# Kernel tuning notes

Measured on AMD Instinct MI355X. Metric: run time of the kernel, lower is better.

Reference implementation:

```python
import jax, jax.numpy as jnp
import numpy as np

B, S, H = 1024, 512, 768
D1, D2 = 128, 1


def setup_inputs() -> dict:
    key = jax.random.key(0)
    k_feat, k_start, k_len, k_w1, k_w2 = jax.random.split(key, 5)
    features_extract = jax.random.normal(k_feat, (B, S, H), dtype=jnp.float32)
    start_token_idx = jax.random.randint(k_start, (B,), 1, 200, dtype=jnp.int64)
    span_len = jax.random.randint(k_len, (B,), 1, 65, dtype=jnp.int64)
    end_token_idx = start_token_idx + span_len  # guaranteed start < end <= 264 < S
    W1 = jax.random.normal(k_w1, (2 * H, D1), dtype=jnp.float32) * (1.0 / np.sqrt(2 * H))
    b1 = jnp.zeros((D1,), dtype=jnp.float32)
    W2 = jax.random.normal(k_w2, (D1, D2), dtype=jnp.float32) * (1.0 / np.sqrt(D1))
    b2 = jnp.zeros((D2,), dtype=jnp.float32)
    return {
        "features_extract": features_extract,
        "start_token_idx": start_token_idx,
        "end_token_idx": end_token_idx,
        "W1": W1, "b1": b1, "W2": W2, "b2": b2,
    }


def reference(features_extract, start_token_idx, end_token_idx, W1, b1, W2, b2):
    # CLS feature: token 0 of each example -> [B, 1, H]
    features_cls = features_extract[:, 0, :][:, None, :]

    # Ragged span mean-pool (vectorized replacement for the per-example loop):
    # mask[b, s] = start[b] <= s < end[b]
    pos = jnp.arange(features_extract.shape[1])  # [S]
    mask = (pos[None, :] >= start_token_idx[:, None]) & (pos[None, :] < end_token_idx[:, None])
    maskf = mask.astype(features_extract.dtype)  # [B, S]
    span_sum = jnp.einsum('bsh,bs->bh', features_extract, maskf)
    span_len = (end_token_idx - start_token_idx).astype(features_extract.dtype)  # >= 1
    features_crc = (span_sum / span_len[:, None])[:, None, :]  # [B, 1, H]

    # Concat + MLP head (dropout layers are identity in eval)
    features = jnp.concatenate([features_cls, features_crc], axis=2)  # [B, 1, 2H]
    h = jax.nn.relu(jnp.einsum('bid,dk->bik', features, W1) + b1)
    out = jax.nn.sigmoid(jnp.einsum('bik,ko->bio', h, W2) + b2)  # [B, 1, 1]
    return out
```

## Files before the change

kernel.cpp:

```cpp
#include <hip/hip_runtime.h>
#include <math.h>

constexpr int Bn = 1024;
constexpr int S  = 512;
constexpr int H  = 768;
constexpr int D1 = 128;
constexpr int HV = H / 4;
constexpr int NH = 512;


__global__ __launch_bounds__(256) void fused_pool_clshead(
    const float* __restrict__ feat, const int* __restrict__ start,
    const int* __restrict__ endp, float* __restrict__ gp,
    const float* __restrict__ W1, float* __restrict__ P) {
  __shared__ __align__(16) char smem[12288];

  const int t = threadIdx.x;

  if (blockIdx.x < NH) {
    float (*g)[384] = reinterpret_cast<float (*)[384]>(smem);
    float (*part)[4][D1] = reinterpret_cast<float (*)[4][D1]>(smem + 6144);

    const int c = blockIdx.x & 1;
    const int e0 = (blockIdx.x >> 1) * 4;
    const int dglob0 = c * 384;

    for (int i = t; i < 384; i += 256) {
      const int e = i / 96;
      const int j = i % 96;
      float4 v = *reinterpret_cast<const float4*>(
          feat + (size_t)(e0 + e) * S * H + dglob0 + j * 4);
      reinterpret_cast<float4*>(&g[e][0])[j] = v;
    }
    __syncthreads();

    const int k = t & (D1 - 1);
    const int sub = t >> 7;
    const int gofs = sub * 192;
    const float* Wc = W1 + (size_t)(dglob0 + gofs) * D1 + k;

    float a0 = 0.f, a1 = 0.f, a2 = 0.f, a3 = 0.f;
    #pragma unroll 4
    for (int d = 0; d < 192; d += 4) {
      float w0 = Wc[(size_t)(d + 0) * D1];
      float w1 = Wc[(size_t)(d + 1) * D1];
      float w2 = Wc[(size_t)(d + 2) * D1];
      float w3 = Wc[(size_t)(d + 3) * D1];
      float4 g0 = *reinterpret_cast<const float4*>(&g[0][gofs + d]);
      float4 g1 = *reinterpret_cast<const float4*>(&g[1][gofs + d]);
      float4 g2 = *reinterpret_cast<const float4*>(&g[2][gofs + d]);
      float4 g3 = *reinterpret_cast<const float4*>(&g[3][gofs + d]);
      a0 += g0.x * w0 + g0.y * w1 + g0.z * w2 + g0.w * w3;
      a1 += g1.x * w0 + g1.y * w1 + g1.z * w2 + g1.w * w3;
      a2 += g2.x * w0 + g2.y * w1 + g2.z * w2 + g2.w * w3;
      a3 += g3.x * w0 + g3.y * w1 + g3.z * w2 + g3.w * w3;
    }
    part[sub][0][k] = a0;
    part[sub][1][k] = a1;
    part[sub][2][k] = a2;
    part[sub][3][k] = a3;
    __syncthreads();

    if (t < D1) {
      #pragma unroll
      for (int e = 0; e < 4; ++e) {
        P[((size_t)c * Bn + (e0 + e)) * D1 + t] = part[0][e][t] + part[1][e][t];
      }
    }
    return;
  }

  {
    float4 (*pacc)[3][64] = reinterpret_cast<float4 (*)[3][64]>(smem);
    const int b = blockIdx.x - NH;
    const int w = t >> 6;
    const int l = t & 63;
    const float4* base =
        reinterpret_cast<const float4*>(feat) + (size_t)b * (S * HV);

    const int s0 = start[b];
    const int s1 = endp[b];

    float4 c0{0,0,0,0}, c1{0,0,0,0}, c2{0,0,0,0};
    float4 d0{0,0,0,0}, d1{0,0,0,0}, d2{0,0,0,0};
    int s = s0 + w;
    for (; s + 4 < s1; s += 8) {
      const float4* r0 = base + (size_t)s * HV;
      const float4* r1 = base + (size_t)(s + 4) * HV;
      float4 u0 = r0[l], u1 = r0[l + 64], u2 = r0[l + 128];
      float4 v0 = r1[l], v1 = r1[l + 64], v2 = r1[l + 128];
      c0.x += u0.x; c0.y += u0.y; c0.z += u0.z; c0.w += u0.w;
      c1.x += u1.x; c1.y += u1.y; c1.z += u1.z; c1.w += u1.w;
      c2.x += u2.x; c2.y += u2.y; c2.z += u2.z; c2.w += u2.w;
      d0.x += v0.x; d0.y += v0.y; d0.z += v0.z; d0.w += v0.w;
      d1.x += v1.x; d1.y += v1.y; d1.z += v1.z; d1.w += v1.w;
      d2.x += v2.x; d2.y += v2.y; d2.z += v2.z; d2.w += v2.w;
    }
    for (; s < s1; s += 4) {
      const float4* r0 = base + (size_t)s * HV;
      float4 u0 = r0[l], u1 = r0[l + 64], u2 = r0[l + 128];
      c0.x += u0.x; c0.y += u0.y; c0.z += u0.z; c0.w += u0.w;
      c1.x += u1.x; c1.y += u1.y; c1.z += u1.z; c1.w += u1.w;
      c2.x += u2.x; c2.y += u2.y; c2.z += u2.z; c2.w += u2.w;
    }
    c0.x += d0.x; c0.y += d0.y; c0.z += d0.z; c0.w += d0.w;
    c1.x += d1.x; c1.y += d1.y; c1.z += d1.z; c1.w += d1.w;
    c2.x += d2.x; c2.y += d2.y; c2.z += d2.z; c2.w += d2.w;
    pacc[w][0][l] = c0;
    pacc[w][1][l] = c1;
    pacc[w][2][l] = c2;
    __syncthreads();

    if (t < 192) {
      const int seg = t >> 6, ln = t & 63;
      float4 a = pacc[0][seg][ln], bb = pacc[1][seg][ln];
      float4 cq = pacc[2][seg][ln], dq = pacc[3][seg][ln];
      const float inv = 1.0f / (float)(s1 - s0);
      float4 r;
      r.x = ((a.x + bb.x) + (cq.x + dq.x)) * inv;
      r.y = ((a.y + bb.y) + (cq.y + dq.y)) * inv;
      r.z = ((a.z + bb.z) + (cq.z + dq.z)) * inv;
      r.w = ((a.w + bb.w) + (cq.w + dq.w)) * inv;
      reinterpret_cast<float4*>(gp)[(size_t)b * HV + t] = r;
    }
  }
}

__global__ __launch_bounds__(256) void crc_head(
    const float* __restrict__ gp, const float* __restrict__ W1,
    float* __restrict__ P) {
  __shared__ float g[4][192];
  __shared__ float part[2][4][D1];

  const int t = threadIdx.x;
  const int cc = blockIdx.x & 3;
  const int e0 = (blockIdx.x >> 2) * 4;
  const int dd04 = cc * 48;

  if (t < 192) {
    const int e = t / 48;
    const int j = t % 48;
    float4 v = reinterpret_cast<const float4*>(gp)[(size_t)(e0 + e) * HV + dd04 + j];
    reinterpret_cast<float4*>(&g[e][0])[j] = v;
  }
  __syncthreads();

  const int k = t & (D1 - 1);
  const int sub = t >> 7;
  const int gofs = sub * 96;
  const float* Wc = W1 + (size_t)(H + cc * 192 + gofs) * D1 + k;

  float a0 = 0.f, a1 = 0.f, a2 = 0.f, a3 = 0.f;
  #pragma unroll 2
  for (int d = 0; d < 96; d += 8) {
    float w0 = Wc[(size_t)(d + 0) * D1];
    float w1 = Wc[(size_t)(d + 1) * D1];
    float w2 = Wc[(size_t)(d + 2) * D1];
    float w3 = Wc[(size_t)(d + 3) * D1];
    float w4 = Wc[(size_t)(d + 4) * D1];
    float w5 = Wc[(size_t)(d + 5) * D1];
    float w6 = Wc[(size_t)(d + 6) * D1];
    float w7 = Wc[(size_t)(d + 7) * D1];
    #define ACC8(i)                                                        \
    {                                                                      \
      float4 gA = *reinterpret_cast<const float4*>(&g[i][gofs + d]);       \
      float4 gB = *reinterpret_cast<const float4*>(&g[i][gofs + d + 4]);   \
      a##i += gA.x * w0 + gA.y * w1 + gA.z * w2 + gA.w * w3                \
            + gB.x * w4 + gB.y * w5 + gB.z * w6 + gB.w * w7;               \
    }
    ACC8(0) ACC8(1) ACC8(2) ACC8(3)
    #undef ACC8
  }
  part[sub][0][k] = a0;
  part[sub][1][k] = a1;
  part[sub][2][k] = a2;
  part[sub][3][k] = a3;
  __syncthreads();

  if (t < D1) {
    #pragma unroll
    for (int e = 0; e < 4; ++e) {
      P[((size_t)(2 + cc) * Bn + (e0 + e)) * D1 + t] =
          part[0][e][t] + part[1][e][t];
    }
  }
}

__global__ __launch_bounds__(256) void finalize(
    const float* __restrict__ P, const float* __restrict__ b1,
    const float* __restrict__ W2, const float* __restrict__ b2,
    float* __restrict__ out) {
  const int t = threadIdx.x;
  const int w = t >> 6, l = t & 63;
  const int e = blockIdx.x * 4 + w;
  const int k0 = l, k1 = l + 64;
  float h0 = b1[k0], h1 = b1[k1];
  #pragma unroll
  for (int c = 0; c < 6; ++c) {
    h0 += P[((size_t)c * Bn + e) * D1 + k0];
    h1 += P[((size_t)c * Bn + e) * D1 + k1];
  }
  h0 = fmaxf(h0, 0.f); h1 = fmaxf(h1, 0.f);
  float v = h0 * W2[k0] + h1 * W2[k1];
  #pragma unroll
  for (int off = 32; off > 0; off >>= 1) v += __shfl_down(v, off);
  if (l == 0) out[e] = 1.0f / (1.0f + expf(-(v + b2[0])));
}

extern "C" void kernel_launch(void* const* d_in, const int* in_sizes, int n_in,
                              void* d_out, int out_size, void* d_ws, size_t ws_size,
                              hipStream_t stream) {
  const float* feat = (const float*)d_in[0];
  const int* start  = (const int*)d_in[1];
  const int* endp   = (const int*)d_in[2];
  const float* W1   = (const float*)d_in[3];
  const float* b1   = (const float*)d_in[4];
  const float* W2   = (const float*)d_in[5];
  const float* b2   = (const float*)d_in[6];
  float* out = (float*)d_out;

  float* wsf = (float*)d_ws;
  float* gp  = wsf;
  float* P   = gp + (size_t)Bn * H;

  hipLaunchKernelGGL(fused_pool_clshead, dim3(NH + Bn), dim3(256), 0,
                     stream, feat, start, endp, gp, W1, P);
  hipLaunchKernelGGL(crc_head, dim3(Bn), dim3(256), 0, stream, gp, W1, P);
  hipLaunchKernelGGL(finalize, dim3(Bn / 4), dim3(256), 0, stream,
                     P, b1, W2, b2, out);
}
```

Measured before the change: 32.85 us.

## Pipeline pooling halves with head and finalize stages across four kernels

Splits the pooling work into two halves by example and co-schedules the second half of pooling with the CRC head for the first half. The CRC head for the second half then runs alongside finalize for the first half, and a last kernel finalizes the rest. The aim is to hide the small, latency-bound head and finalize kernels behind bandwidth-bound pooling instead of running them serially. The cost is an extra kernel launch and some load imbalance between the mixed block types.

Result: slower. 36.44 us (+10.9%).

```diff
diff --git a/kernel.cpp b/kernel.cpp
--- a/kernel.cpp
+++ b/kernel.cpp
@@ -6,141 +6,135 @@
 constexpr int H  = 768;
 constexpr int D1 = 128;
 constexpr int HV = H / 4;
-constexpr int NH = 512;
-
-
-__global__ __launch_bounds__(256) void fused_pool_clshead(
+constexpr int HALF = 512;
+
+
+
+__device__ __forceinline__ void cls_head_fn(
+    const float* __restrict__ feat, const float* __restrict__ W1,
+    float* __restrict__ P, int bid, int t, char* smem) {
+  float (*g)[384] = reinterpret_cast<float (*)[384]>(smem);
+  float (*part)[4][D1] = reinterpret_cast<float (*)[4][D1]>(smem + 6144);
+
+  const int c = bid & 1;
+  const int e0 = (bid >> 1) * 4;
+  const int dglob0 = c * 384;
+
+  for (int i = t; i < 384; i += 256) {
+    const int e = i / 96;
+    const int j = i % 96;
+    float4 v = *reinterpret_cast<const float4*>(
+        feat + (size_t)(e0 + e) * S * H + dglob0 + j * 4);
+    reinterpret_cast<float4*>(&g[e][0])[j] = v;
+  }
+  __syncthreads();
+
+  const int k = t & (D1 - 1);
+  const int sub = t >> 7;
+  const int gofs = sub * 192;
+  const float* Wc = W1 + (size_t)(dglob0 + gofs) * D1 + k;
+
+  float a0 = 0.f, a1 = 0.f, a2 = 0.f, a3 = 0.f;
+  #pragma unroll 4
+  for (int d = 0; d < 192; d += 4) {
+    float w0 = Wc[(size_t)(d + 0) * D1];
+    float w1 = Wc[(size_t)(d + 1) * D1];
+    float w2 = Wc[(size_t)(d + 2) * D1];
+    float w3 = Wc[(size_t)(d + 3) * D1];
+    float4 g0 = *reinterpret_cast<const float4*>(&g[0][gofs + d]);
+    float4 g1 = *reinterpret_cast<const float4*>(&g[1][gofs + d]);
+    float4 g2 = *reinterpret_cast<const float4*>(&g[2][gofs + d]);
+    float4 g3 = *reinterpret_cast<const float4*>(&g[3][gofs + d]);
+    a0 += g0.x * w0 + g0.y * w1 + g0.z * w2 + g0.w * w3;
+    a1 += g1.x * w0 + g1.y * w1 + g1.z * w2 + g1.w * w3;
+    a2 += g2.x * w0 + g2.y * w1 + g2.z * w2 + g2.w * w3;
+    a3 += g3.x * w0 + g3.y * w1 + g3.z * w2 + g3.w * w3;
+  }
+  part[sub][0][k] = a0;
+  part[sub][1][k] = a1;
+  part[sub][2][k] = a2;
+  part[sub][3][k] = a3;
+  __syncthreads();
+
+  if (t < D1) {
+    #pragma unroll
+    for (int e = 0; e < 4; ++e) {
+      P[((size_t)c * Bn + (e0 + e)) * D1 + t] = part[0][e][t] + part[1][e][t];
+    }
+  }
+}
+
+__device__ __forceinline__ void pool_fn(
     const float* __restrict__ feat, const int* __restrict__ start,
-    const int* __restrict__ endp, float* __restrict__ gp,
-    const float* __restrict__ W1, float* __restrict__ P) {
-  __shared__ __align__(16) char smem[12288];
-
-  const int t = threadIdx.x;
-
-  if (blockIdx.x < NH) {
-    float (*g)[384] = reinterpret_cast<float (*)[384]>(smem);
-    float (*part)[4][D1] = reinterpret_cast<float (*)[4][D1]>(smem + 6144);
-
-    const int c = blockIdx.x & 1;
-    const int e0 = (blockIdx.x >> 1) * 4;
-    const int dglob0 = c * 384;
-
-    for (int i = t; i < 384; i += 256) {
-      const int e = i / 96;
-      const int j = i % 96;
-      float4 v = *reinterpret_cast<const float4*>(
-          feat + (size_t)(e0 + e) * S * H + dglob0 + j * 4);
-      reinterpret_cast<float4*>(&g[e][0])[j] = v;
-    }
-    __syncthreads();
-
-    const int k = t & (D1 - 1);
-    const int sub = t >> 7;
-    const int gofs = sub * 192;
-    const float* Wc = W1 + (size_t)(dglob0 + gofs) * D1 + k;
-
-    float a0 = 0.f, a1 = 0.f, a2 = 0.f, a3 = 0.f;
-    #pragma unroll 4
-    for (int d = 0; d < 192; d += 4) {
-      float w0 = Wc[(size_t)(d + 0) * D1];
-      float w1 = Wc[(size_t)(d + 1) * D1];
-      float w2 = Wc[(size_t)(d + 2) * D1];
-      float w3 = Wc[(size_t)(d + 3) * D1];
-      float4 g0 = *reinterpret_cast<const float4*>(&g[0][gofs + d]);
-      float4 g1 = *reinterpret_cast<const float4*>(&g[1][gofs + d]);
-      float4 g2 = *reinterpret_cast<const float4*>(&g[2][gofs + d]);
-      float4 g3 = *reinterpret_cast<const float4*>(&g[3][gofs + d]);
-      a0 += g0.x * w0 + g0.y * w1 + g0.z * w2 + g0.w * w3;
-      a1 += g1.x * w0 + g1.y * w1 + g1.z * w2 + g1.w * w3;
-      a2 += g2.x * w0 + g2.y * w1 + g2.z * w2 + g2.w * w3;
-      a3 += g3.x * w0 + g3.y * w1 + g3.z * w2 + g3.w * w3;
-    }
-    part[sub][0][k] = a0;
-    part[sub][1][k] = a1;
-    part[sub][2][k] = a2;
-    part[sub][3][k] = a3;
-    __syncthreads();
-
-    if (t < D1) {
-      #pragma unroll
-      for (int e = 0; e < 4; ++e) {
-        P[((size_t)c * Bn + (e0 + e)) * D1 + t] = part[0][e][t] + part[1][e][t];
-      }
-    }
-    return;
-  }
-
-  {
-    float4 (*pacc)[3][64] = reinterpret_cast<float4 (*)[3][64]>(smem);
-    const int b = blockIdx.x - NH;
-    const int w = t >> 6;
-    const int l = t & 63;
-    const float4* base =
-        reinterpret_cast<const float4*>(feat) + (size_t)b * (S * HV);
-
-    const int s0 = start[b];
-    const int s1 = endp[b];
-
-    float4 c0{0,0,0,0}, c1{0,0,0,0}, c2{0,0,0,0};
-    float4 d0{0,0,0,0}, d1{0,0,0,0}, d2{0,0,0,0};
-    int s = s0 + w;
-    for (; s + 4 < s1; s += 8) {
-      const float4* r0 = base + (size_t)s * HV;
-      const float4* r1 = base + (size_t)(s + 4) * HV;
-      float4 u0 = r0[l], u1 = r0[l + 64], u2 = r0[l + 128];
-      float4 v0 = r1[l], v1 = r1[l + 64], v2 = r1[l + 128];
-      c0.x += u0.x; c0.y += u0.y; c0.z += u0.z; c0.w += u0.w;
-      c1.x += u1.x; c1.y += u1.y; c1.z += u1.z; c1.w += u1.w;
-      c2.x += u2.x; c2.y += u2.y; c2.z += u2.z; c2.w += u2.w;
-      d0.x += v0.x; d0.y += v0.y; d0.z += v0.z; d0.w += v0.w;
-      d1.x += v1.x; d1.y += v1.y; d1.z += v1.z; d1.w += v1.w;
-      d2.x += v2.x; d2.y += v2.y; d2.z += v2.z; d2.w += v2.w;
-    }
-    for (; s < s1; s += 4) {
-      const float4* r0 = base + (size_t)s * HV;
-      float4 u0 = r0[l], u1 = r0[l + 64], u2 = r0[l + 128];
-      c0.x += u0.x; c0.y += u0.y; c0.z += u0.z; c0.w += u0.w;
-      c1.x += u1.x; c1.y += u1.y; c1.z += u1.z; c1.w += u1.w;
-      c2.x += u2.x; c2.y += u2.y; c2.z += u2.z; c2.w += u2.w;
-    }
-    c0.x += d0.x; c0.y += d0.y; c0.z += d0.z; c0.w += d0.w;
-    c1.x += d1.x; c1.y += d1.y; c1.z += d1.z; c1.w += d1.w;
-    c2.x += d2.x; c2.y += d2.y; c2.z += d2.z; c2.w += d2.w;
-    pacc[w][0][l] = c0;
-    pacc[w][1][l] = c1;
-    pacc[w][2][l] = c2;
-    __syncthreads();
-
-    if (t < 192) {
-      const int seg = t >> 6, ln = t & 63;
-      float4 a = pacc[0][seg][ln], bb = pacc[1][seg][ln];
-      float4 cq = pacc[2][seg][ln], dq = pacc[3][seg][ln];
-      const float inv = 1.0f / (float)(s1 - s0);
-      float4 r;
-      r.x = ((a.x + bb.x) + (cq.x + dq.x)) * inv;
-      r.y = ((a.y + bb.y) + (cq.y + dq.y)) * inv;
-      r.z = ((a.z + bb.z) + (cq.z + dq.z)) * inv;
-      r.w = ((a.w + bb.w) + (cq.w + dq.w)) * inv;
-      reinterpret_cast<float4*>(gp)[(size_t)b * HV + t] = r;
-    }
-  }
-}
-
-__global__ __launch_bounds__(256) void crc_head(
+    const int* __restrict__ endp, float* __restrict__ gp, int b, int t,
+    char* smem) {
+  float4 (*pacc)[3][64] = reinterpret_cast<float4 (*)[3][64]>(smem);
+  const int w = t >> 6;
+  const int l = t & 63;
+  const float4* base =
+      reinterpret_cast<const float4*>(feat) + (size_t)b * (S * HV);
+
+  const int s0 = start[b];
+  const int s1 = endp[b];
+
+  float4 c0{0,0,0,0}, c1{0,0,0,0}, c2{0,0,0,0};
+  float4 d0{0,0,0,0}, d1{0,0,0,0}, d2{0,0,0,0};
+  int s = s0 + w;
+  for (; s + 4 < s1; s += 8) {
+    const float4* r0 = base + (size_t)s * HV;
+    const float4* r1 = base + (size_t)(s + 4) * HV;
+    float4 u0 = r0[l], u1 = r0[l + 64], u2 = r0[l + 128];
+    float4 v0 = r1[l], v1 = r1[l + 64], v2 = r1[l + 128];
+    c0.x += u0.x; c0.y += u0.y; c0.z += u0.z; c0.w += u0.w;
+    c1.x += u1.x; c1.y += u1.y; c1.z += u1.z; c1.w += u1.w;
+    c2.x += u2.x; c2.y += u2.y; c2.z += u2.z; c2.w += u2.w;
+    d0.x += v0.x; d0.y += v0.y; d0.z += v0.z; d0.w += v0.w;
+    d1.x += v1.x; d1.y += v1.y; d1.z += v1.z; d1.w += v1.w;
+    d2.x += v2.x; d2.y += v2.y; d2.z += v2.z; d2.w += v2.w;
+  }
+  for (; s < s1; s += 4) {
+    const float4* r0 = base + (size_t)s * HV;
+    float4 u0 = r0[l], u1 = r0[l + 64], u2 = r0[l + 128];
+    c0.x += u0.x; c0.y += u0.y; c0.z += u0.z; c0.w += u0.w;
+    c1.x += u1.x; c1.y += u1.y; c1.z += u1.z; c1.w += u1.w;
+    c2.x += u2.x; c2.y += u2.y; c2.z += u2.z; c2.w += u2.w;
+  }
+  c0.x += d0.x; c0.y += d0.y; c0.z += d0.z; c0.w += d0.w;
+  c1.x += d1.x; c1.y += d1.y; c1.z += d1.z; c1.w += d1.w;
+  c2.x += d2.x; c2.y += d2.y; c2.z += d2.z; c2.w += d2.w;
+  pacc[w][0][l] = c0;
+  pacc[w][1][l] = c1;
+  pacc[w][2][l] = c2;
+  __syncthreads();
+
+  if (t < 192) {
+    const int seg = t >> 6, ln = t & 63;
+    float4 a = pacc[0][seg][ln], bb = pacc[1][seg][ln];
+    float4 cq = pacc[2][seg][ln], dq = pacc[3][seg][ln];
+    const float inv = 1.0f / (float)(s1 - s0);
+    float4 r;
+    r.x = ((a.x + bb.x) + (cq.x + dq.x)) * inv;
+    r.y = ((a.y + bb.y) + (cq.y + dq.y)) * inv;
+    r.z = ((a.z + bb.z) + (cq.z + dq.z)) * inv;
+    r.w = ((a.w + bb.w) + (cq.w + dq.w)) * inv;
+    reinterpret_cast<float4*>(gp)[(size_t)b * HV + t] = r;
+  }
+}
+
+__device__ __forceinline__ void crc_fn(
     const float* __restrict__ gp, const float* __restrict__ W1,
-    float* __restrict__ P) {
-  __shared__ float g[4][192];
-  __shared__ float part[2][4][D1];
-
-  const int t = threadIdx.x;
-  const int cc = blockIdx.x & 3;
-  const int e0 = (blockIdx.x >> 2) * 4;
+    float* __restrict__ P, int cc, int eg, int t, char* smem) {
+  float (*g)[192] = reinterpret_cast<float (*)[192]>(smem);
+  float (*part)[4][D1] = reinterpret_cast<float (*)[4][D1]>(smem + 3072);
+
+  const int e0 = eg * 4;
   const int dd04 = cc * 48;
 
   if (t < 192) {
     const int e = t / 48;
     const int j = t % 48;
-    float4 v = reinterpret_cast<const float4*>(gp)[(size_t)(e0 + e) * HV + dd04 + j];
+    float4 v =
+        reinterpret_cast<const float4*>(gp)[(size_t)(e0 + e) * HV + dd04 + j];
     reinterpret_cast<float4*>(&g[e][0])[j] = v;
   }
   __syncthreads();
@@ -186,13 +180,12 @@
   }
 }
 
-__global__ __launch_bounds__(256) void finalize(
+__device__ __forceinline__ void fin_fn(
     const float* __restrict__ P, const float* __restrict__ b1,
     const float* __restrict__ W2, const float* __restrict__ b2,
-    float* __restrict__ out) {
-  const int t = threadIdx.x;
+    float* __restrict__ out, int e0, int t) {
   const int w = t >> 6, l = t & 63;
-  const int e = blockIdx.x * 4 + w;
+  const int e = e0 + w;
   const int k0 = l, k1 = l + 64;
   float h0 = b1[k0], h1 = b1[k1];
   #pragma unroll
@@ -205,6 +198,53 @@
   #pragma unroll
   for (int off = 32; off > 0; off >>= 1) v += __shfl_down(v, off);
   if (l == 0) out[e] = 1.0f / (1.0f + expf(-(v + b2[0])));
+}
+
+
+__global__ __launch_bounds__(256) void stage1(
+    const float* __restrict__ feat, const int* __restrict__ start,
+    const int* __restrict__ endp, float* __restrict__ gp,
+    const float* __restrict__ W1, float* __restrict__ P) {
+  __shared__ __align__(16) char smem[12288];
+  if (blockIdx.x < 512) {
+    cls_head_fn(feat, W1, P, blockIdx.x, threadIdx.x, smem);
+  } else {
+    pool_fn(feat, start, endp, gp, blockIdx.x - 512, threadIdx.x, smem);
+  }
+}
+
+__global__ __launch_bounds__(256) void stage2(
+    const float* __restrict__ feat, const int* __restrict__ start,
+    const int* __restrict__ endp, float* __restrict__ gp,
+    const float* __restrict__ W1, float* __restrict__ P) {
+  __shared__ __align__(16) char smem[12288];
+  if (blockIdx.x < 512) {
+    crc_fn(gp, W1, P, blockIdx.x & 3, blockIdx.x >> 2, threadIdx.x, smem);
+  } else {
+    pool_fn(feat, start, endp, gp, (blockIdx.x - 512) + HALF, threadIdx.x,
+            smem);
+  }
+}
+
+__global__ __launch_bounds__(256) void stage3(
+    const float* __restrict__ gp, const float* __restrict__ W1,
+    float* __restrict__ P, const float* __restrict__ b1,
+    const float* __restrict__ W2, const float* __restrict__ b2,
+    float* __restrict__ out) {
+  __shared__ __align__(16) char smem[12288];
+  if (blockIdx.x < 512) {
+    crc_fn(gp, W1, P, blockIdx.x & 3, (blockIdx.x >> 2) + HALF / 4,
+           threadIdx.x, smem);
+  } else {
+    fin_fn(P, b1, W2, b2, out, (blockIdx.x - 512) * 4, threadIdx.x);
+  }
+}
+
+__global__ __launch_bounds__(256) void stage4(
+    const float* __restrict__ P, const float* __restrict__ b1,
+    const float* __restrict__ W2, const float* __restrict__ b2,
+    float* __restrict__ out) {
+  fin_fn(P, b1, W2, b2, out, HALF + blockIdx.x * 4, threadIdx.x);
 }
 
 extern "C" void kernel_launch(void* const* d_in, const int* in_sizes, int n_in,
@@ -223,9 +263,12 @@
   float* gp  = wsf;
   float* P   = gp + (size_t)Bn * H;
 
-  hipLaunchKernelGGL(fused_pool_clshead, dim3(NH + Bn), dim3(256), 0,
-                     stream, feat, start, endp, gp, W1, P);
-  hipLaunchKernelGGL(crc_head, dim3(Bn), dim3(256), 0, stream, gp, W1, P);
-  hipLaunchKernelGGL(finalize, dim3(Bn / 4), dim3(256), 0, stream,
+  hipLaunchKernelGGL(stage1, dim3(1024), dim3(256), 0, stream,
+                     feat, start, endp, gp, W1, P);
+  hipLaunchKernelGGL(stage2, dim3(1024), dim3(256), 0, stream,
+                     feat, start, endp, gp, W1, P);
+  hipLaunchKernelGGL(stage3, dim3(640), dim3(256), 0, stream,
+                     gp, W1, P, b1, W2, b2, out);
+  hipLaunchKernelGGL(stage4, dim3(128), dim3(256), 0, stream,
                      P, b1, W2, b2, out);
 }
```

## Split span pooling across three blocks per example along hidden dim

Applied to the files above, without the earlier changes.

The span mean-pool work for each example now runs in three blocks, each covering 64 float4 columns of the hidden dimension, instead of one block covering all 192. The inner loop loads one float4 per row with four-way row unrolling over four independent accumulators, and shared memory shrinks. This triples the pooling block count so more loads are in flight across the GPU for short ragged spans, at the cost of more block launches and repeated start/end index reads.

After: 34.03 us. 3.6% more time.

```diff
diff --git a/kernel.cpp b/kernel.cpp
--- a/kernel.cpp
+++ b/kernel.cpp
@@ -13,7 +13,7 @@
     const float* __restrict__ feat, const int* __restrict__ start,
     const int* __restrict__ endp, float* __restrict__ gp,
     const float* __restrict__ W1, float* __restrict__ P) {
-  __shared__ __align__(16) char smem[12288];
+  __shared__ __align__(16) char smem[10240];
 
   const int t = threadIdx.x;
 
@@ -71,57 +71,52 @@
   }
 
   {
-    float4 (*pacc)[3][64] = reinterpret_cast<float4 (*)[3][64]>(smem);
-    const int b = blockIdx.x - NH;
+    float4 (*pacc)[64] = reinterpret_cast<float4 (*)[64]>(smem);
+    const int bb = blockIdx.x - NH;
+    const int b = bb / 3;
+    const int p = bb - b * 3;
     const int w = t >> 6;
     const int l = t & 63;
-    const float4* base =
-        reinterpret_cast<const float4*>(feat) + (size_t)b * (S * HV);
+
+    const float4* base4 =
+        reinterpret_cast<const float4*>(feat) + (size_t)b * (S * HV) + p * 64;
 
     const int s0 = start[b];
     const int s1 = endp[b];
 
-    float4 c0{0,0,0,0}, c1{0,0,0,0}, c2{0,0,0,0};
-    float4 d0{0,0,0,0}, d1{0,0,0,0}, d2{0,0,0,0};
+    float4 a0{0,0,0,0}, a1{0,0,0,0}, a2{0,0,0,0}, a3{0,0,0,0};
     int s = s0 + w;
-    for (; s + 4 < s1; s += 8) {
-      const float4* r0 = base + (size_t)s * HV;
-      const float4* r1 = base + (size_t)(s + 4) * HV;
-      float4 u0 = r0[l], u1 = r0[l + 64], u2 = r0[l + 128];
-      float4 v0 = r1[l], v1 = r1[l + 64], v2 = r1[l + 128];
-      c0.x += u0.x; c0.y += u0.y; c0.z += u0.z; c0.w += u0.w;
-      c1.x += u1.x; c1.y += u1.y; c1.z += u1.z; c1.w += u1.w;
-      c2.x += u2.x; c2.y += u2.y; c2.z += u2.z; c2.w += u2.w;
-      d0.x += v0.x; d0.y += v0.y; d0.z += v0.z; d0.w += v0.w;
-      d1.x += v1.x; d1.y += v1.y; d1.z += v1.z; d1.w += v1.w;
-      d2.x += v2.x; d2.y += v2.y; d2.z += v2.z; d2.w += v2.w;
+    for (; s + 12 < s1; s += 16) {
+      float4 v0 = base4[(size_t)(s +  0) * HV + l];
+      float4 v1 = base4[(size_t)(s +  4) * HV + l];
+      float4 v2 = base4[(size_t)(s +  8) * HV + l];
+      float4 v3 = base4[(size_t)(s + 12) * HV + l];
+      a0.x += v0.x; a0.y += v0.y; a0.z += v0.z; a0.w += v0.w;
+      a1.x += v1.x; a1.y += v1.y; a1.z += v1.z; a1.w += v1.w;
+      a2.x += v2.x; a2.y += v2.y; a2.z += v2.z; a2.w += v2.w;
+      a3.x += v3.x; a3.y += v3.y; a3.z += v3.z; a3.w += v3.w;
     }
     for (; s < s1; s += 4) {
-      const float4* r0 = base + (size_t)s * HV;
-      float4 u0 = r0[l], u1 = r0[l + 64], u2 = r0[l + 128];
-      c0.x += u0.x; c0.y += u0.y; c0.z += u0.z; c0.w += u0.w;
-      c1.x += u1.x; c1.y += u1.y; c1.z += u1.z; c1.w += u1.w;
-      c2.x += u2.x; c2.y += u2.y; c2.z += u2.z; c2.w += u2.w;
-    }
-    c0.x += d0.x; c0.y += d0.y; c0.z += d0.z; c0.w += d0.w;
-    c1.x += d1.x; c1.y += d1.y; c1.z += d1.z; c1.w += d1.w;
-    c2.x += d2.x; c2.y += d2.y; c2.z += d2.z; c2.w += d2.w;
-    pacc[w][0][l] = c0;
-    pacc[w][1][l] = c1;
-    pacc[w][2][l] = c2;
+      float4 v = base4[(size_t)s * HV + l];
+      a0.x += v.x; a0.y += v.y; a0.z += v.z; a0.w += v.w;
+    }
+    float4 r;
+    r.x = (a0.x + a1.x) + (a2.x + a3.x);
+    r.y = (a0.y + a1.y) + (a2.y + a3.y);
+    r.z = (a0.z + a1.z) + (a2.z + a3.z);
+    r.w = (a0.w + a1.w) + (a2.w + a3.w);
+    pacc[w][l] = r;
     __syncthreads();
 
-    if (t < 192) {
-      const int seg = t >> 6, ln = t & 63;
-      float4 a = pacc[0][seg][ln], bb = pacc[1][seg][ln];
-      float4 cq = pacc[2][seg][ln], dq = pacc[3][seg][ln];
+    if (t < 64) {
       const float inv = 1.0f / (float)(s1 - s0);
-      float4 r;
-      r.x = ((a.x + bb.x) + (cq.x + dq.x)) * inv;
-      r.y = ((a.y + bb.y) + (cq.y + dq.y)) * inv;
-      r.z = ((a.z + bb.z) + (cq.z + dq.z)) * inv;
-      r.w = ((a.w + bb.w) + (cq.w + dq.w)) * inv;
-      reinterpret_cast<float4*>(gp)[(size_t)b * HV + t] = r;
+      float4 q0 = pacc[0][t], q1 = pacc[1][t], q2 = pacc[2][t], q3 = pacc[3][t];
+      float4 o;
+      o.x = ((q0.x + q1.x) + (q2.x + q3.x)) * inv;
+      o.y = ((q0.y + q1.y) + (q2.y + q3.y)) * inv;
+      o.z = ((q0.z + q1.z) + (q2.z + q3.z)) * inv;
+      o.w = ((q0.w + q1.w) + (q2.w + q3.w)) * inv;
+      reinterpret_cast<float4*>(gp)[(size_t)b * HV + p * 64 + t] = o;
     }
   }
 }
@@ -223,7 +218,7 @@
   float* gp  = wsf;
   float* P   = gp + (size_t)Bn * H;
 
-  hipLaunchKernelGGL(fused_pool_clshead, dim3(NH + Bn), dim3(256), 0,
+  hipLaunchKernelGGL(fused_pool_clshead, dim3(NH + 3 * Bn), dim3(256), 0,
                      stream, feat, start, endp, gp, W1, P);
   hipLaunchKernelGGL(crc_head, dim3(Bn), dim3(256), 0, stream, gp, W1, P);
   hipLaunchKernelGGL(finalize, dim3(Bn / 4), dim3(256), 0, stream,
```
